# Optimization experiments

Measured on AMD Instinct MI355X. Metric: run time of the kernel, lower is better.

The kernel has to match this reference:

```python
import jax, jax.numpy as jnp
import numpy as np

N_NODES = 100000
N_EDGES = 1600000
F_IN, HIDDEN, N_CLASS = 64, 48, 40


def setup_inputs() -> dict:
    key = jax.random.key(0)
    ks = jax.random.split(key, 9)
    def glorot(k, fi, fo):
        s = (6.0 / (fi + fo)) ** 0.5
        return jax.random.uniform(k, (fi, fo), jnp.float32, -s, s)
    return {
        "x": jax.random.normal(ks[0], (N_NODES, F_IN), jnp.float32),
        "edge_index": jax.random.randint(ks[1], (2, N_EDGES), 0, N_NODES, jnp.int64),
        "edge_weight": jax.random.uniform(ks[2], (N_EDGES,), jnp.float32),
        "W1": glorot(ks[3], F_IN, HIDDEN),   # ARMAConv init_weight (K=1)
        "V1": glorot(ks[4], F_IN, HIDDEN),   # ARMAConv root_weight
        "b1": jnp.zeros((HIDDEN,), jnp.float32),
        "W2": glorot(ks[5], HIDDEN, N_CLASS),
        "V2": glorot(ks[6], HIDDEN, N_CLASS),
        "b2": jnp.zeros((N_CLASS,), jnp.float32),
    }


def _arma_conv(x, W, V, b, src, dst, norm, num_nodes):
    # out = ReLU( A_norm @ (x @ W) + x @ V + b )   (num_stacks=1, num_layers=1)
    h = x @ W                                   # [N, F_out]
    msg = h[src] * norm[:, None]                # gather + scale  [E, F_out]
    agg = jax.ops.segment_sum(msg, dst, num_segments=num_nodes)  # scatter-add
    return jax.nn.relu(agg + x @ V + b)


def reference(x, edge_index, edge_weight, W1, V1, b1, W2, V2, b2):
    num_nodes = x.shape[0]
    src, dst = edge_index[0], edge_index[1]
    # gcn_norm, add_self_loops=False: D^{-1/2} A D^{-1/2}
    deg = jax.ops.segment_sum(edge_weight, dst, num_segments=num_nodes)
    dinv = jnp.where(deg > 0, jax.lax.rsqrt(jnp.where(deg > 0, deg, 1.0)), 0.0)
    norm = dinv[src] * edge_weight * dinv[dst]
    # eval mode: input dropout is identity
    h = _arma_conv(x, W1, V1, b1, src, dst, norm, num_nodes)
    h = _arma_conv(h, W2, V2, b2, src, dst, norm, num_nodes)
    return jax.nn.log_softmax(h, axis=-1)
```

## Files before the change

### kernel.cpp

```cpp
#include <hip/hip_runtime.h>
#include <math.h>


constexpr int F_IN = 64;
constexpr int HIDDEN = 48;
constexpr int N_CLASS = 40;
constexpr int CHUNK = 8192;
constexpr int BIN_SHIFT = 9;
constexpr int CSR_CAP = 12288;

typedef __attribute__((ext_vector_type(8))) short bf16x8;
typedef __attribute__((ext_vector_type(4))) float f32x4;

__device__ __forceinline__ short bfr(float f) {
    unsigned u = __float_as_uint(f);
    return (short)((u + 0x7fffu + ((u >> 16) & 1u)) >> 16);
}
__device__ __forceinline__ unsigned pack_bf2(float a, float b) {
    unsigned ua = __float_as_uint(a), ub = __float_as_uint(b);
    ua = (ua + 0x7fffu + ((ua >> 16) & 1u)) >> 16;
    ub = (ub + 0x7fffu + ((ub >> 16) & 1u)) >> 16;
    return ua | (ub << 16);
}
__device__ __forceinline__ float2 unpack_bf2(unsigned u) {
    return make_float2(__uint_as_float(u << 16), __uint_as_float(u & 0xffff0000u));
}
__device__ __forceinline__ bf16x8 cvt8(float4 f0, float4 f1) {
    bf16x8 r;
    r[0] = bfr(f0.x); r[1] = bfr(f0.y); r[2] = bfr(f0.z); r[3] = bfr(f0.w);
    r[4] = bfr(f1.x); r[5] = bfr(f1.y); r[6] = bfr(f1.z); r[7] = bfr(f1.w);
    return r;
}

__device__ __forceinline__ void mfma_gemm1_body(char* smem, const float* __restrict__ X,
                                                const float* __restrict__ W,
                                                const float* __restrict__ V,
                                                const float* __restrict__ b,
                                                unsigned* __restrict__ XWp,
                                                float* __restrict__ AGG, int N, int gb,
                                                int tid) {
    short* sWT = (short*)smem;
    float* ep = (float*)(smem + 12288);
    for (int i = tid; i < 96 * 64; i += 256) {
        int c = i >> 6, k = i & 63;
        float v = (c < 48) ? W[k * 48 + c] : V[k * 48 + (c - 48)];
        sWT[i] = bfr(v);
    }
    __syncthreads();

    int lane = tid & 63, wv = tid >> 6;
    int m = lane & 15, quad = lane >> 4;
    int nb0 = gb * 64;
    int n = nb0 + wv * 16 + m;

    bf16x8 a0, a1;
    if (n < N) {
        const float4* xr = (const float4*)(X + (size_t)n * 64 + quad * 8);
        a0 = cvt8(xr[0], xr[1]);
        const float4* xr2 = (const float4*)(X + (size_t)n * 64 + 32 + quad * 8);
        a1 = cvt8(xr2[0], xr2[1]);
    } else {
        for (int j = 0; j < 8; ++j) { a0[j] = 0; a1[j] = 0; }
    }

    f32x4 acc[6];
#pragma unroll
    for (int ct = 0; ct < 6; ++ct) acc[ct] = (f32x4){0.f, 0.f, 0.f, 0.f};
#pragma unroll
    for (int ct = 0; ct < 6; ++ct) {
        bf16x8 b0 = *(const bf16x8*)(sWT + (ct * 16 + m) * 64 + quad * 8);
        bf16x8 b1 = *(const bf16x8*)(sWT + (ct * 16 + m) * 64 + 32 + quad * 8);
        acc[ct] = __builtin_amdgcn_mfma_f32_16x16x32_bf16(a0, b0, acc[ct], 0, 0, 0);
        acc[ct] = __builtin_amdgcn_mfma_f32_16x16x32_bf16(a1, b1, acc[ct], 0, 0, 0);
    }
#pragma unroll
    for (int ct = 0; ct < 6; ++ct)
#pragma unroll
        for (int r = 0; r < 4; ++r)
            ep[(wv * 16 + quad * 4 + r) * 96 + ct * 16 + m] = acc[ct][r];
    __syncthreads();
    for (int i = tid; i < 64 * 24; i += 256) {
        int r = i / 24, c2 = i - r * 24;
        int node = nb0 + r;
        if (node >= N) continue;
        float w0 = ep[r * 96 + 2 * c2], w1 = ep[r * 96 + 2 * c2 + 1];
        XWp[node * 24 + c2] = pack_bf2(w0, w1);
        float v0 = ep[r * 96 + 48 + 2 * c2], v1 = ep[r * 96 + 48 + 2 * c2 + 1];
        float2 bb = ((const float2*)b)[c2];
        ((float2*)AGG)[node * 24 + c2] = make_float2(v0 + bb.x, v1 + bb.y);
    }
}

__global__ __launch_bounds__(256) void count_gemm1(
    const int* __restrict__ dst, int* __restrict__ binCnt, int E, int nCountBlocks,
    const float* __restrict__ X, const float* __restrict__ W,
    const float* __restrict__ V, const float* __restrict__ b,
    unsigned* __restrict__ XWp, float* __restrict__ AGG, int N) {
    __shared__ char smem[36864];
    if ((int)blockIdx.x < nCountBlocks) {
        int* hist = (int*)smem;
        int tid = threadIdx.x;
        hist[tid] = 0;
        __syncthreads();
        long long e0 = (long long)blockIdx.x * CHUNK;
        int M = (int)min((long long)CHUNK, (long long)E - e0);
        for (int i = tid; i < M; i += 256) atomicAdd(&hist[dst[e0 + i] >> BIN_SHIFT], 1);
        __syncthreads();
        atomicAdd(&binCnt[tid], hist[tid]);
    } else {
        mfma_gemm1_body(smem, X, W, V, b, XWp, AGG, N,
                        (int)blockIdx.x - nCountBlocks, (int)threadIdx.x);
    }
}

__global__ void scan_bins(const int* __restrict__ binCnt, int* __restrict__ binStart,
                          int* __restrict__ binCursor, int* __restrict__ rowPtr,
                          int E, int N) {
    __shared__ int s[256];
    int t = threadIdx.x;
    int v = binCnt[t];
    s[t] = v;
    __syncthreads();
#pragma unroll
    for (int o = 1; o < 256; o <<= 1) {
        int u = (t >= o) ? s[t - o] : 0;
        __syncthreads();
        s[t] += u;
        __syncthreads();
    }
    int excl = s[t] - v;
    binStart[t] = excl;
    binCursor[t] = excl;
    if (t == 0) {
        binStart[256] = E;
        rowPtr[N] = E;
    }
}

__global__ void binscatter(const int* __restrict__ src, const int* __restrict__ dst,
                           const float* __restrict__ w, int* __restrict__ binCursor,
                           int2* __restrict__ binned, int E) {
    __shared__ int sx[CHUNK];
    __shared__ int sw[CHUNK];
    __shared__ unsigned char sbin[CHUNK];
    __shared__ int hist[256];
    int tid = threadIdx.x;
    hist[tid] = 0;
    __syncthreads();
    long long e0 = (long long)blockIdx.x * CHUNK;
    int M = (int)min((long long)CHUNK, (long long)E - e0);
    for (int i = tid; i < M; i += 256) {
        int d = dst[e0 + i];
        int bn = d >> BIN_SHIFT;
        sx[i] = ((d & 511) << 17) | src[e0 + i];
        sw[i] = __float_as_int(w[e0 + i]);
        sbin[i] = (unsigned char)bn;
        atomicAdd(&hist[bn], 1);
    }
    __syncthreads();
    int base = atomicAdd(&binCursor[tid], hist[tid]);
    __syncthreads();
    hist[tid] = base;
    __syncthreads();
    for (int i = tid; i < M; i += 256) {
        int p = atomicAdd(&hist[sbin[i]], 1);
        binned[p] = make_int2(sx[i], sw[i]);
    }
}

__global__ __launch_bounds__(512) void build_csr(const int2* __restrict__ binned,
                                                 const int* __restrict__ binStart,
                                                 int* __restrict__ rowPtr,
                                                 float* __restrict__ dinv,
                                                 unsigned* __restrict__ csr, int N) {
    __shared__ int sx[CSR_CAP];
    __shared__ int sw[CSR_CAP];
    __shared__ int cntL[512];
    __shared__ float degL[512];
    __shared__ int scanL[512];
    int b = blockIdx.x, tid = threadIdx.x;
    int e0 = binStart[b], e1 = binStart[b + 1], M = e1 - e0;
    cntL[tid] = 0;
    degL[tid] = 0.f;
    __syncthreads();
    bool fits = (M <= CSR_CAP);
    for (int i = tid; i < M; i += 512) {
        int2 p = binned[e0 + i];
        if (fits) { sx[i] = p.x; sw[i] = p.y; }
        int dl = ((unsigned)p.x) >> 17;
        atomicAdd(&cntL[dl], 1);
        atomicAdd(&degL[dl], __int_as_float(p.y));
    }
    __syncthreads();
    int v = cntL[tid];
    scanL[tid] = v;
    __syncthreads();
#pragma unroll
    for (int o = 1; o < 512; o <<= 1) {
        int u = (tid >= o) ? scanL[tid - o] : 0;
        __syncthreads();
        scanL[tid] += u;
        __syncthreads();
    }
    int excl = scanL[tid] - v;
    int node = (b << BIN_SHIFT) + tid;
    float dg = degL[tid];
    float dv = dg > 0.f ? rsqrtf(dg) : 0.f;
    if (node < N) {
        rowPtr[node] = e0 + excl;
        dinv[node] = dv;
    }
    cntL[tid] = e0 + excl;
    degL[tid] = dv;
    __syncthreads();
    for (int i = tid; i < M; i += 512) {
        int px, pw;
        if (fits) { px = sx[i]; pw = sw[i]; }
        else { int2 p = binned[e0 + i]; px = p.x; pw = p.y; }
        int dl = ((unsigned)px) >> 17;
        int pos = atomicAdd(&cntL[dl], 1);
        float wn = __int_as_float(pw) * degL[dl];
        unsigned uw = __float_as_uint(wn);
        uw = (uw + 0x7fffu + ((uw >> 16) & 1u)) >> 16;
        csr[pos] = ((unsigned)(px & 0x1FFFF) << 15) | uw;
    }
}

__global__ void scale_xw(unsigned* __restrict__ XWp, const float* __restrict__ dinv,
                         int total) {
    int t = blockIdx.x * blockDim.x + threadIdx.x;
    if (t >= total) return;
    float dv = dinv[t / 24];
    float2 u = unpack_bf2(XWp[t]);
    XWp[t] = pack_bf2(u.x * dv, u.y * dv);
}

template <int W>
__device__ __forceinline__ float2 row_accumC(const unsigned* __restrict__ XWp,
                                             const unsigned* __restrict__ csr, int j,
                                             int end, int c, float2 s) {
    for (; j + 4 <= end; j += 4) {
        unsigned p0 = csr[j], p1 = csr[j + 1], p2 = csr[j + 2], p3 = csr[j + 3];
        unsigned u0 = XWp[(p0 >> 15) * W + c];
        unsigned u1 = XWp[(p1 >> 15) * W + c];
        unsigned u2 = XWp[(p2 >> 15) * W + c];
        unsigned u3 = XWp[(p3 >> 15) * W + c];
        float2 x0 = unpack_bf2(u0), x1 = unpack_bf2(u1);
        float2 x2 = unpack_bf2(u2), x3 = unpack_bf2(u3);
        float n0 = __uint_as_float((p0 & 0x7FFFu) << 16);
        float n1 = __uint_as_float((p1 & 0x7FFFu) << 16);
        float n2 = __uint_as_float((p2 & 0x7FFFu) << 16);
        float n3 = __uint_as_float((p3 & 0x7FFFu) << 16);
        s.x = fmaf(x0.x, n0, s.x); s.y = fmaf(x0.y, n0, s.y);
        s.x = fmaf(x1.x, n1, s.x); s.y = fmaf(x1.y, n1, s.y);
        s.x = fmaf(x2.x, n2, s.x); s.y = fmaf(x2.y, n2, s.y);
        s.x = fmaf(x3.x, n3, s.x); s.y = fmaf(x3.y, n3, s.y);
    }
    for (; j < end; ++j) {
        unsigned p = csr[j];
        float2 xw = unpack_bf2(XWp[(p >> 15) * W + c]);
        float nr = __uint_as_float((p & 0x7FFFu) << 16);
        s.x = fmaf(xw.x, nr, s.x);
        s.y = fmaf(xw.y, nr, s.y);
    }
    return s;
}

__global__ void pull_agg(const unsigned* __restrict__ XWp, const unsigned* __restrict__ csr,
                         const int* __restrict__ rowPtr, const float* __restrict__ AGGin,
                         unsigned* __restrict__ H1p, int N) {
    constexpr int C2 = HIDDEN / 2;
    int t = blockIdx.x * blockDim.x + threadIdx.x;
    if (t >= N * C2) return;
    int n = t / C2, c2 = t - n * C2;
    float2 s = ((const float2*)AGGin)[t];
    s = row_accumC<C2>(XWp, csr, rowPtr[n], rowPtr[n + 1], c2, s);
    H1p[t] = pack_bf2(fmaxf(s.x, 0.f), fmaxf(s.y, 0.f));
}

__global__ __launch_bounds__(256) void gemm2_kernel(
    const short* __restrict__ H1, const float* __restrict__ W,
    const float* __restrict__ V, const float* __restrict__ b,
    const float* __restrict__ dinv, unsigned* __restrict__ XWp,
    float* __restrict__ AGG, int N) {
    __shared__ char smem[30720];
    short* sWT = (short*)smem;
    float* ep = (float*)(smem + 10240);
    int tid = threadIdx.x;
    for (int i = tid; i < 80 * 64; i += 256) {
        int c = i >> 6, k = i & 63;
        float v = 0.f;
        if (k < 48) v = (c < 40) ? W[k * 40 + c] : V[k * 40 + (c - 40)];
        sWT[i] = bfr(v);
    }
    __syncthreads();

    int lane = tid & 63, wv = tid >> 6;
    int m = lane & 15, quad = lane >> 4;
    int nb0 = (int)blockIdx.x * 64;
    int n = nb0 + wv * 16 + m;

    bf16x8 a0, a1;
    if (n < N) {
        a0 = *(const bf16x8*)(H1 + (size_t)n * 48 + quad * 8);
        if (quad < 2) {
            a1 = *(const bf16x8*)(H1 + (size_t)n * 48 + 32 + quad * 8);
        } else {
            for (int j = 0; j < 8; ++j) a1[j] = 0;
        }
    } else {
        for (int j = 0; j < 8; ++j) { a0[j] = 0; a1[j] = 0; }
    }

    f32x4 acc[5];
#pragma unroll
    for (int ct = 0; ct < 5; ++ct) acc[ct] = (f32x4){0.f, 0.f, 0.f, 0.f};
#pragma unroll
    for (int ct = 0; ct < 5; ++ct) {
        bf16x8 b0 = *(const bf16x8*)(sWT + (ct * 16 + m) * 64 + quad * 8);
        bf16x8 b1 = *(const bf16x8*)(sWT + (ct * 16 + m) * 64 + 32 + quad * 8);
        acc[ct] = __builtin_amdgcn_mfma_f32_16x16x32_bf16(a0, b0, acc[ct], 0, 0, 0);
        acc[ct] = __builtin_amdgcn_mfma_f32_16x16x32_bf16(a1, b1, acc[ct], 0, 0, 0);
    }
#pragma unroll
    for (int ct = 0; ct < 5; ++ct)
#pragma unroll
        for (int r = 0; r < 4; ++r)
            ep[(wv * 16 + quad * 4 + r) * 80 + ct * 16 + m] = acc[ct][r];
    __syncthreads();
    for (int i = tid; i < 64 * 20; i += 256) {
        int r = i / 20, c2 = i - r * 20;
        int node = nb0 + r;
        if (node >= N) continue;
        float dv = dinv[node];
        float w0 = ep[r * 80 + 2 * c2], w1 = ep[r * 80 + 2 * c2 + 1];
        XWp[node * 20 + c2] = pack_bf2(w0 * dv, w1 * dv);
        float v0 = ep[r * 80 + 40 + 2 * c2], v1 = ep[r * 80 + 40 + 2 * c2 + 1];
        float2 bb = ((const float2*)b)[c2];
        ((float2*)AGG)[node * 20 + c2] = make_float2(v0 + bb.x, v1 + bb.y);
    }
}

__global__ __launch_bounds__(320) void pull_ls(const unsigned* __restrict__ XWp,
                                               const unsigned* __restrict__ csr,
                                               const int* __restrict__ rowPtr,
                                               const float* __restrict__ AGGin,
                                               float* __restrict__ out, int N) {
    constexpr int C2 = N_CLASS / 2;
    __shared__ float2 sbuf[16 * C2];
    __shared__ float sl[16];
    int tid = threadIdx.x;
    int nl = tid / C2, c2 = tid - nl * C2;
    int n = blockIdx.x * 16 + nl;
    float2 s = make_float2(0.f, 0.f);
    if (n < N) {
        s = ((const float2*)AGGin)[n * C2 + c2];
        s = row_accumC<C2>(XWp, csr, rowPtr[n], rowPtr[n + 1], c2, s);
    }
    sbuf[tid] = s;
    __syncthreads();
    if (tid < 16) {
        const float2* row = sbuf + tid * C2;
        float m = 0.f;
        for (int k = 0; k < C2; ++k) {
            float2 v = row[k];
            m = fmaxf(m, fmaxf(v.x, v.y));
        }
        float sum = 0.f;
        for (int k = 0; k < C2; ++k) {
            float2 v = row[k];
            sum += expf(fmaxf(v.x, 0.f) - m) + expf(fmaxf(v.y, 0.f) - m);
        }
        sl[tid] = m + logf(sum);
    }
    __syncthreads();
    if (n < N) {
        float l = sl[nl];
        ((float2*)out)[n * C2 + c2] =
            make_float2(fmaxf(s.x, 0.f) - l, fmaxf(s.y, 0.f) - l);
    }
}

extern "C" void kernel_launch(void* const* d_in, const int* in_sizes, int n_in,
                              void* d_out, int out_size, void* d_ws, size_t ws_size,
                              hipStream_t stream) {
    const float* x  = (const float*)d_in[0];
    const int*   ei = (const int*)d_in[1];
    const float* ew = (const float*)d_in[2];
    const float* W1 = (const float*)d_in[3];
    const float* V1 = (const float*)d_in[4];
    const float* b1 = (const float*)d_in[5];
    const float* W2 = (const float*)d_in[6];
    const float* V2 = (const float*)d_in[7];
    const float* b2 = (const float*)d_in[8];
    float* out = (float*)d_out;

    const int N = in_sizes[0] / F_IN;
    const int E = in_sizes[2];
    const int* src = ei;
    const int* dst = ei + E;

    char* ws = (char*)d_ws;
    size_t off = 0;
    auto carve = [&](size_t bytes) {
        void* p = ws + off;
        off = (off + bytes + 255) & ~size_t(255);
        return p;
    };
    int*      binCnt    = (int*)carve(256 * 4);
    int*      binStart  = (int*)carve(257 * 4);
    int*      binCursor = (int*)carve(256 * 4);
    int*      rowPtr    = (int*)carve((size_t)(N + 1) * 4);
    float*    dinv      = (float*)carve((size_t)N * 4);
    int2*     binned    = (int2*)carve((size_t)E * 8);
    unsigned* csr       = (unsigned*)carve((size_t)E * 4);
    unsigned* xW1p      = (unsigned*)carve((size_t)N * 24 * 4);
    float*    agg1      = (float*)carve((size_t)N * HIDDEN * 4);
    unsigned* h1p       = (unsigned*)carve((size_t)N * 24 * 4);
    unsigned* xW2p      = (unsigned*)carve((size_t)N * 20 * 4);
    float*    agg2      = (float*)carve((size_t)N * N_CLASS * 4);

    const int B = 256;
    auto cdiv = [](long long a, long long b) { return (int)((a + b - 1) / b); };
    const int nChunks = cdiv(E, CHUNK);
    const int nBins = (N + (1 << BIN_SHIFT) - 1) >> BIN_SHIFT;
    const int nGemmBlocks = cdiv(N, 64);

    hipMemsetAsync(binCnt, 0, 256 * 4, stream);

    count_gemm1<<<nChunks + nGemmBlocks, B, 0, stream>>>(dst, binCnt, E, nChunks,
                                                         x, W1, V1, b1, xW1p, agg1, N);
    scan_bins<<<1, 256, 0, stream>>>(binCnt, binStart, binCursor, rowPtr, E, N);
    binscatter<<<nChunks, B, 0, stream>>>(src, dst, ew, binCursor, binned, E);
    build_csr<<<nBins, 512, 0, stream>>>(binned, binStart, rowPtr, dinv, csr, N);

    scale_xw<<<cdiv((long long)N * 24, B), B, 0, stream>>>(xW1p, dinv, N * 24);

    pull_agg<<<cdiv((long long)N * 24, B), B, 0, stream>>>(xW1p, csr, rowPtr,
                                                           agg1, h1p, N);

    gemm2_kernel<<<nGemmBlocks, B, 0, stream>>>((const short*)h1p, W2, V2, b2,
                                                dinv, xW2p, agg2, N);

    pull_ls<<<cdiv(N, 16), 320, 0, stream>>>(xW2p, csr, rowPtr, agg2, out, N);
}
```

Baseline: 287.0 us.

## Widen pull-aggregation to 4 features per thread and store root terms in bf16

The pull-aggregation kernels now handle four features per thread instead of two, using 8-byte gathers of packed bf16 neighbor rows and 16-byte vector loads of the CSR after an alignment prologue. This halves the number of threads that re-read each row's CSR entries. The x@V+b root terms are stored as packed bf16 instead of fp32, which halves their write and read traffic at some cost in precision. Launch configurations change to match: 384-thread blocks for layer 1 and 32 nodes per block for the log-softmax kernel.

```diff
diff --git a/kernel.cpp b/kernel.cpp
--- a/kernel.cpp
+++ b/kernel.cpp
@@ -37,8 +37,8 @@
                                                 const float* __restrict__ V,
                                                 const float* __restrict__ b,
                                                 unsigned* __restrict__ XWp,
-                                                float* __restrict__ AGG, int N, int gb,
-                                                int tid) {
+                                                unsigned* __restrict__ AGGp, int N,
+                                                int gb, int tid) {
     short* sWT = (short*)smem;
     float* ep = (float*)(smem + 12288);
     for (int i = tid; i < 96 * 64; i += 256) {
@@ -87,7 +87,7 @@
         XWp[node * 24 + c2] = pack_bf2(w0, w1);
         float v0 = ep[r * 96 + 48 + 2 * c2], v1 = ep[r * 96 + 48 + 2 * c2 + 1];
         float2 bb = ((const float2*)b)[c2];
-        ((float2*)AGG)[node * 24 + c2] = make_float2(v0 + bb.x, v1 + bb.y);
+        AGGp[node * 24 + c2] = pack_bf2(v0 + bb.x, v1 + bb.y);
     }
 }
 
@@ -95,7 +95,7 @@
     const int* __restrict__ dst, int* __restrict__ binCnt, int E, int nCountBlocks,
     const float* __restrict__ X, const float* __restrict__ W,
     const float* __restrict__ V, const float* __restrict__ b,
-    unsigned* __restrict__ XWp, float* __restrict__ AGG, int N) {
+    unsigned* __restrict__ XWp, unsigned* __restrict__ AGGp, int N) {
     __shared__ char smem[36864];
     if ((int)blockIdx.x < nCountBlocks) {
         int* hist = (int*)smem;
@@ -108,7 +108,7 @@
         __syncthreads();
         atomicAdd(&binCnt[tid], hist[tid]);
     } else {
-        mfma_gemm1_body(smem, X, W, V, b, XWp, AGG, N,
+        mfma_gemm1_body(smem, X, W, V, b, XWp, AGGp, N,
                         (int)blockIdx.x - nCountBlocks, (int)threadIdx.x);
     }
 }
@@ -236,53 +236,75 @@
 }
 
 template <int W>
-__device__ __forceinline__ float2 row_accumC(const unsigned* __restrict__ XWp,
-                                             const unsigned* __restrict__ csr, int j,
-                                             int end, int c, float2 s) {
+__device__ __forceinline__ float4 row_accum2(const unsigned* __restrict__ XWp,
+                                             const unsigned* __restrict__ csr,
+                                             int j, int end, int c, float4 s) {
+    while (j < end && (j & 3)) {
+        unsigned p = csr[j++];
+        uint2 u = *(const uint2*)(XWp + (p >> 15) * W + c);
+        float nr = __uint_as_float((p & 0x7FFFu) << 16);
+        float2 x0 = unpack_bf2(u.x), x1 = unpack_bf2(u.y);
+        s.x = fmaf(x0.x, nr, s.x); s.y = fmaf(x0.y, nr, s.y);
+        s.z = fmaf(x1.x, nr, s.z); s.w = fmaf(x1.y, nr, s.w);
+    }
     for (; j + 4 <= end; j += 4) {
-        unsigned p0 = csr[j], p1 = csr[j + 1], p2 = csr[j + 2], p3 = csr[j + 3];
-        unsigned u0 = XWp[(p0 >> 15) * W + c];
-        unsigned u1 = XWp[(p1 >> 15) * W + c];
-        unsigned u2 = XWp[(p2 >> 15) * W + c];
-        unsigned u3 = XWp[(p3 >> 15) * W + c];
-        float2 x0 = unpack_bf2(u0), x1 = unpack_bf2(u1);
-        float2 x2 = unpack_bf2(u2), x3 = unpack_bf2(u3);
-        float n0 = __uint_as_float((p0 & 0x7FFFu) << 16);
-        float n1 = __uint_as_float((p1 & 0x7FFFu) << 16);
-        float n2 = __uint_as_float((p2 & 0x7FFFu) << 16);
-        float n3 = __uint_as_float((p3 & 0x7FFFu) << 16);
-        s.x = fmaf(x0.x, n0, s.x); s.y = fmaf(x0.y, n0, s.y);
-        s.x = fmaf(x1.x, n1, s.x); s.y = fmaf(x1.y, n1, s.y);
-        s.x = fmaf(x2.x, n2, s.x); s.y = fmaf(x2.y, n2, s.y);
-        s.x = fmaf(x3.x, n3, s.x); s.y = fmaf(x3.y, n3, s.y);
+        uint4 p4 = *(const uint4*)(csr + j);
+        uint2 u0 = *(const uint2*)(XWp + (p4.x >> 15) * W + c);
+        uint2 u1 = *(const uint2*)(XWp + (p4.y >> 15) * W + c);
+        uint2 u2 = *(const uint2*)(XWp + (p4.z >> 15) * W + c);
+        uint2 u3 = *(const uint2*)(XWp + (p4.w >> 15) * W + c);
+        float n0 = __uint_as_float((p4.x & 0x7FFFu) << 16);
+        float n1 = __uint_as_float((p4.y & 0x7FFFu) << 16);
+        float n2 = __uint_as_float((p4.z & 0x7FFFu) << 16);
+        float n3 = __uint_as_float((p4.w & 0x7FFFu) << 16);
+        float2 a0 = unpack_bf2(u0.x), b0 = unpack_bf2(u0.y);
+        float2 a1 = unpack_bf2(u1.x), b1 = unpack_bf2(u1.y);
+        float2 a2 = unpack_bf2(u2.x), b2 = unpack_bf2(u2.y);
+        float2 a3 = unpack_bf2(u3.x), b3 = unpack_bf2(u3.y);
+        s.x = fmaf(a0.x, n0, s.x); s.y = fmaf(a0.y, n0, s.y);
+        s.z = fmaf(b0.x, n0, s.z); s.w = fmaf(b0.y, n0, s.w);
+        s.x = fmaf(a1.x, n1, s.x); s.y = fmaf(a1.y, n1, s.y);
+        s.z = fmaf(b1.x, n1, s.z); s.w = fmaf(b1.y, n1, s.w);
+        s.x = fmaf(a2.x, n2, s.x); s.y = fmaf(a2.y, n2, s.y);
+        s.z = fmaf(b2.x, n2, s.z); s.w = fmaf(b2.y, n2, s.w);
+        s.x = fmaf(a3.x, n3, s.x); s.y = fmaf(a3.y, n3, s.y);
+        s.z = fmaf(b3.x, n3, s.z); s.w = fmaf(b3.y, n3, s.w);
     }
     for (; j < end; ++j) {
         unsigned p = csr[j];
-        float2 xw = unpack_bf2(XWp[(p >> 15) * W + c]);
+        uint2 u = *(const uint2*)(XWp + (p >> 15) * W + c);
         float nr = __uint_as_float((p & 0x7FFFu) << 16);
-        s.x = fmaf(xw.x, nr, s.x);
-        s.y = fmaf(xw.y, nr, s.y);
+        float2 x0 = unpack_bf2(u.x), x1 = unpack_bf2(u.y);
+        s.x = fmaf(x0.x, nr, s.x); s.y = fmaf(x0.y, nr, s.y);
+        s.z = fmaf(x1.x, nr, s.z); s.w = fmaf(x1.y, nr, s.w);
     }
     return s;
 }
 
-__global__ void pull_agg(const unsigned* __restrict__ XWp, const unsigned* __restrict__ csr,
-                         const int* __restrict__ rowPtr, const float* __restrict__ AGGin,
-                         unsigned* __restrict__ H1p, int N) {
-    constexpr int C2 = HIDDEN / 2;
+__global__ __launch_bounds__(384) void pull_agg(const unsigned* __restrict__ XWp,
+                                                const unsigned* __restrict__ csr,
+                                                const int* __restrict__ rowPtr,
+                                                const unsigned* __restrict__ AGG1p,
+                                                unsigned* __restrict__ H1p, int N) {
     int t = blockIdx.x * blockDim.x + threadIdx.x;
-    if (t >= N * C2) return;
-    int n = t / C2, c2 = t - n * C2;
-    float2 s = ((const float2*)AGGin)[t];
-    s = row_accumC<C2>(XWp, csr, rowPtr[n], rowPtr[n + 1], c2, s);
-    H1p[t] = pack_bf2(fmaxf(s.x, 0.f), fmaxf(s.y, 0.f));
+    int n = t / 12, c1 = t - n * 12;
+    if (n >= N) return;
+    int c = 2 * c1;
+    uint2 a = *(const uint2*)(AGG1p + n * 24 + c);
+    float2 f0 = unpack_bf2(a.x), f1 = unpack_bf2(a.y);
+    float4 s = make_float4(f0.x, f0.y, f1.x, f1.y);
+    s = row_accum2<24>(XWp, csr, rowPtr[n], rowPtr[n + 1], c, s);
+    uint2 o;
+    o.x = pack_bf2(fmaxf(s.x, 0.f), fmaxf(s.y, 0.f));
+    o.y = pack_bf2(fmaxf(s.z, 0.f), fmaxf(s.w, 0.f));
+    *(uint2*)(H1p + n * 24 + c) = o;
 }
 
 __global__ __launch_bounds__(256) void gemm2_kernel(
     const short* __restrict__ H1, const float* __restrict__ W,
     const float* __restrict__ V, const float* __restrict__ b,
     const float* __restrict__ dinv, unsigned* __restrict__ XWp,
-    float* __restrict__ AGG, int N) {
+    unsigned* __restrict__ AGGp, int N) {
     __shared__ char smem[30720];
     short* sWT = (short*)smem;
     float* ep = (float*)(smem + 10240);
@@ -337,47 +359,50 @@
         XWp[node * 20 + c2] = pack_bf2(w0 * dv, w1 * dv);
         float v0 = ep[r * 80 + 40 + 2 * c2], v1 = ep[r * 80 + 40 + 2 * c2 + 1];
         float2 bb = ((const float2*)b)[c2];
-        ((float2*)AGG)[node * 20 + c2] = make_float2(v0 + bb.x, v1 + bb.y);
+        AGGp[node * 20 + c2] = pack_bf2(v0 + bb.x, v1 + bb.y);
     }
 }
 
 __global__ __launch_bounds__(320) void pull_ls(const unsigned* __restrict__ XWp,
                                                const unsigned* __restrict__ csr,
                                                const int* __restrict__ rowPtr,
-                                               const float* __restrict__ AGGin,
+                                               const unsigned* __restrict__ AGG2p,
                                                float* __restrict__ out, int N) {
-    constexpr int C2 = N_CLASS / 2;
-    __shared__ float2 sbuf[16 * C2];
-    __shared__ float sl[16];
+    __shared__ float4 sbuf[32 * 10];
+    __shared__ float sl[32];
     int tid = threadIdx.x;
-    int nl = tid / C2, c2 = tid - nl * C2;
-    int n = blockIdx.x * 16 + nl;
-    float2 s = make_float2(0.f, 0.f);
+    int nl = tid / 10, c1 = tid - nl * 10;
+    int n = blockIdx.x * 32 + nl;
+    int c = 2 * c1;
+    float4 s = make_float4(0.f, 0.f, 0.f, 0.f);
     if (n < N) {
-        s = ((const float2*)AGGin)[n * C2 + c2];
-        s = row_accumC<C2>(XWp, csr, rowPtr[n], rowPtr[n + 1], c2, s);
-    }
-    sbuf[tid] = s;
-    __syncthreads();
-    if (tid < 16) {
-        const float2* row = sbuf + tid * C2;
+        uint2 a = *(const uint2*)(AGG2p + n * 20 + c);
+        float2 f0 = unpack_bf2(a.x), f1 = unpack_bf2(a.y);
+        s = make_float4(f0.x, f0.y, f1.x, f1.y);
+        s = row_accum2<20>(XWp, csr, rowPtr[n], rowPtr[n + 1], c, s);
+    }
+    sbuf[nl * 10 + c1] = s;
+    __syncthreads();
+    if (tid < 32) {
         float m = 0.f;
-        for (int k = 0; k < C2; ++k) {
-            float2 v = row[k];
-            m = fmaxf(m, fmaxf(v.x, v.y));
+        for (int k = 0; k < 10; ++k) {
+            float4 v = sbuf[tid * 10 + k];
+            m = fmaxf(m, fmaxf(fmaxf(v.x, v.y), fmaxf(v.z, v.w)));
         }
         float sum = 0.f;
-        for (int k = 0; k < C2; ++k) {
-            float2 v = row[k];
-            sum += expf(fmaxf(v.x, 0.f) - m) + expf(fmaxf(v.y, 0.f) - m);
+        for (int k = 0; k < 10; ++k) {
+            float4 v = sbuf[tid * 10 + k];
+            sum += expf(fmaxf(v.x, 0.f) - m) + expf(fmaxf(v.y, 0.f) - m) +
+                   expf(fmaxf(v.z, 0.f) - m) + expf(fmaxf(v.w, 0.f) - m);
         }
         sl[tid] = m + logf(sum);
     }
     __syncthreads();
     if (n < N) {
         float l = sl[nl];
-        ((float2*)out)[n * C2 + c2] =
-            make_float2(fmaxf(s.x, 0.f) - l, fmaxf(s.y, 0.f) - l);
+        ((float4*)out)[n * 10 + c1] =
+            make_float4(fmaxf(s.x, 0.f) - l, fmaxf(s.y, 0.f) - l,
+                        fmaxf(s.z, 0.f) - l, fmaxf(s.w, 0.f) - l);
     }
 }
 
@@ -415,10 +440,10 @@
     int2*     binned    = (int2*)carve((size_t)E * 8);
     unsigned* csr       = (unsigned*)carve((size_t)E * 4);
     unsigned* xW1p      = (unsigned*)carve((size_t)N * 24 * 4);
-    float*    agg1      = (float*)carve((size_t)N * HIDDEN * 4);
+    unsigned* agg1p     = (unsigned*)carve((size_t)N * 24 * 4);
     unsigned* h1p       = (unsigned*)carve((size_t)N * 24 * 4);
     unsigned* xW2p      = (unsigned*)carve((size_t)N * 20 * 4);
-    float*    agg2      = (float*)carve((size_t)N * N_CLASS * 4);
+    unsigned* agg2p     = (unsigned*)carve((size_t)N * 20 * 4);
 
     const int B = 256;
     auto cdiv = [](long long a, long long b) { return (int)((a + b - 1) / b); };
@@ -429,18 +454,18 @@
     hipMemsetAsync(binCnt, 0, 256 * 4, stream);
 
     count_gemm1<<<nChunks + nGemmBlocks, B, 0, stream>>>(dst, binCnt, E, nChunks,
-                                                         x, W1, V1, b1, xW1p, agg1, N);
+                                                         x, W1, V1, b1, xW1p, agg1p, N);
     scan_bins<<<1, 256, 0, stream>>>(binCnt, binStart, binCursor, rowPtr, E, N);
     binscatter<<<nChunks, B, 0, stream>>>(src, dst, ew, binCursor, binned, E);
     build_csr<<<nBins, 512, 0, stream>>>(binned, binStart, rowPtr, dinv, csr, N);
 
     scale_xw<<<cdiv((long long)N * 24, B), B, 0, stream>>>(xW1p, dinv, N * 24);
 
-    pull_agg<<<cdiv((long long)N * 24, B), B, 0, stream>>>(xW1p, csr, rowPtr,
-                                                           agg1, h1p, N);
+    pull_agg<<<cdiv((long long)N * 12, 384), 384, 0, stream>>>(xW1p, csr, rowPtr,
+                                                               agg1p, h1p, N);
 
     gemm2_kernel<<<nGemmBlocks, B, 0, stream>>>((const short*)h1p, W2, V2, b2,
-                                                dinv, xW2p, agg2, N);
-
-    pull_ls<<<cdiv(N, 16), 320, 0, stream>>>(xW2p, csr, rowPtr, agg2, out, N);
-}
+                                                dinv, xW2p, agg2p, N);
+
+    pull_ls<<<cdiv(N, 32), 320, 0, stream>>>(xW2p, csr, rowPtr, agg2p, out, N);
+}
```

New measurement: 278.3 us. 1.03x faster.
